# Kernel optimization log

Hardware: AMD Instinct MI355X
Metric: run time of the kernel (lower is better)

The kernel has to match this reference:

```python
import jax, jax.numpy as jnp
import numpy as np

N, E, DIN, HID, DOUT = 50000, 800000, 128, 128, 64
NEG_SLOPE = 0.2


def setup_inputs() -> dict:
    key = jax.random.key(0)
    ks = jax.random.split(key, 16)
    x = jax.random.normal(ks[0], (N, DIN), dtype=jnp.float32)
    edge_index = jax.random.randint(ks[1], (2, E), 0, N, dtype=jnp.int64)

    def lin(k, fan_in, fan_out):
        kw, kb = jax.random.split(k)
        s = 1.0 / np.sqrt(fan_in)
        W = jax.random.uniform(kw, (fan_in, fan_out), jnp.float32, -s, s)
        b = jax.random.uniform(kb, (fan_out,), jnp.float32, -s, s)
        return W, b

    Wl, bl = lin(ks[2], DIN, DIN)   # GATv2 lin_l
    Wr, br = lin(ks[3], DIN, DIN)   # GATv2 lin_r
    att = jax.random.uniform(ks[4], (DIN,), jnp.float32, -1.0 / np.sqrt(DIN), 1.0 / np.sqrt(DIN))
    bg = jnp.zeros((DIN,), jnp.float32)  # GAT output bias
    W1, b1 = lin(ks[5], DIN, HID)   # ChebConv K=1 -> plain linear
    W2, b2 = lin(ks[6], HID, HID)
    W3, b3 = lin(ks[7], HID, DOUT)
    return {"x": x, "edge_index": edge_index, "Wl": Wl, "bl": bl, "Wr": Wr,
            "br": br, "att": att, "bg": bg, "W1": W1, "b1": b1,
            "W2": W2, "b2": b2, "W3": W3, "b3": b3}


def reference(x, edge_index, Wl, bl, Wr, br, att, bg, W1, b1, W2, b2, W3, b3):
    n = x.shape[0]
    # GATv2Conv adds self loops by default
    loop = jnp.arange(n, dtype=edge_index.dtype)
    src = jnp.concatenate([edge_index[0], loop])  # source j
    dst = jnp.concatenate([edge_index[1], loop])  # target i

    xl = x @ Wl + bl  # [N, DIN]
    xr = x @ Wr + br  # [N, DIN]

    # GATv2 edge scores: leaky_relu(x_l[j] + x_r[i]) . att
    e = jax.nn.leaky_relu(xl[src] + xr[dst], NEG_SLOPE)  # [E+N, DIN]
    a = e @ att                                          # [E+N]

    # softmax over incoming edges of each destination node
    amax = jax.ops.segment_max(a, dst, num_segments=n)
    ea = jnp.exp(a - amax[dst])
    denom = jax.ops.segment_sum(ea, dst, num_segments=n)
    alpha = ea / denom[dst]                              # [E+N]

    # aggregate messages alpha * x_l[j] at destinations
    h = jax.ops.segment_sum(alpha[:, None] * xl[src], dst, num_segments=n) + bg

    # ChebConv with K=1 reduces to a linear layer (T_0(L) = I)
    h = jax.nn.relu(h @ W1 + b1)
    h = jax.nn.relu(h @ W2 + b2)
    # dropout_rate = 0.0 -> identity
    return h @ W3 + b3
```

## Files before the change

### kernel.cpp

```cpp
#include <hip/hip_runtime.h>
#include <hip/hip_bf16.h>

#define DIN 128
#define NEG_SLOPE 0.2f
#define PTILE 4096
#define PAD 64
#define SPAD 4608
#define CVT_BLKS 289

typedef __attribute__((ext_vector_type(8))) short bf16x8;
typedef __attribute__((ext_vector_type(8))) unsigned short u16x8;
typedef __attribute__((ext_vector_type(4))) float f32x4;
typedef __attribute__((ext_vector_type(2))) float f32x2;
typedef __attribute__((ext_vector_type(4))) unsigned int u32x4;

__device__ __forceinline__ ushort f2bf(float f) {
  unsigned u = __float_as_uint(f);
  u += 0x7FFFu + ((u >> 16) & 1u);
  return (ushort)(u >> 16);
}
__device__ __forceinline__ float bf2f(ushort u) {
  return __uint_as_float((unsigned)u << 16);
}
__device__ __forceinline__ f32x2 bfpair(unsigned u) {
  f32x2 r;
  r.x = __uint_as_float(u << 16);
  r.y = __uint_as_float(u & 0xFFFF0000u);
  return r;
}

template <int CTRL>
__device__ __forceinline__ float dppadd(float x) {
  int v = __builtin_amdgcn_update_dpp(0, __float_as_int(x), CTRL, 0xf, 0xf, true);
  return x + __int_as_float(v);
}
__device__ __forceinline__ float red16(float t) {
  t = dppadd<0xB1>(t);
  t = dppadd<0x4E>(t);
  t = dppadd<0x141>(t);
  t = dppadd<0x140>(t);
  return t;
}

__global__ __launch_bounds__(256) void part_cvt_kernel(
    const int* __restrict__ ei, unsigned* __restrict__ part,
    int* __restrict__ cnt2, int ntile, int E,
    const float* __restrict__ Wl, const float* __restrict__ Wr,
    const float* __restrict__ W1, const float* __restrict__ W2,
    const float* __restrict__ W3,
    ushort* __restrict__ WlT, ushort* __restrict__ WrT,
    ushort* __restrict__ W1T, ushort* __restrict__ W2T,
    ushort* __restrict__ W3T) {
  if ((int)blockIdx.x < ntile) {
    __shared__ int hist[256], pref[256], sexcl[256], curs[256];
    __shared__ unsigned buf[PTILE];
    const int tid = threadIdx.x;
    const int t = blockIdx.x;
    const int tile0 = t * PTILE;
    const int tcount = min(PTILE, E - tile0);
    hist[tid] = 0;
    __syncthreads();
    unsigned pk[PTILE / 256];
    int cnt = 0;
    for (int i = tid; i < tcount; i += 256) {
      int s = ei[tile0 + i], d = ei[E + tile0 + i];
      unsigned p = ((unsigned)d << 16) | (unsigned)s;
      pk[cnt++] = p;
      atomicAdd(&hist[d >> 8], 1);
    }
    __syncthreads();
    int v = hist[tid];
    pref[tid] = v;
    __syncthreads();
    for (int d = 1; d < 256; d <<= 1) {
      int tt = (tid >= d) ? pref[tid - d] : 0;
      __syncthreads();
      pref[tid] += tt;
      __syncthreads();
    }
    int exc = pref[tid] - v;
    sexcl[tid] = exc;
    curs[tid] = exc;
    cnt2[tid * ntile + t] = v;
    __syncthreads();
    for (int j = 0; j < cnt; j++) {
      int b = pk[j] >> 24;
      int pos = atomicAdd(&curs[b], 1);
      buf[pos] = pk[j];
    }
    __syncthreads();
    for (int i = tid; i < tcount; i += 256) {
      unsigned p = buf[i];
      int b = p >> 24;
      int r = i - sexcl[b];
      if (r < PAD)
        part[((long)b * ntile + t) * PAD + r] = p;
    }
  } else {
    int i = ((int)blockIdx.x - ntile) * 256 + threadIdx.x;
    if (i < 16384) {
      int k = i >> 7, c = i & 127; WlT[c * 128 + k] = f2bf(Wl[i]);
    } else if (i < 32768) {
      int j = i - 16384; int k = j >> 7, c = j & 127; WrT[c * 128 + k] = f2bf(Wr[j]);
    } else if (i < 49152) {
      int j = i - 32768; int k = j >> 7, c = j & 127; W1T[c * 128 + k] = f2bf(W1[j]);
    } else if (i < 65536) {
      int j = i - 49152; int k = j >> 7, c = j & 127; W2T[c * 128 + k] = f2bf(W2[j]);
    } else if (i < 73728) {
      int j = i - 65536; int k = j >> 6, c = j & 63; W3T[c * 128 + k] = f2bf(W3[j]);
    }
  }
}

#define XSP 136
__global__ __launch_bounds__(1024) void lin_fine_kernel(
    const float* __restrict__ x, const float* __restrict__ att,
    const ushort* __restrict__ WlT, const float* __restrict__ bl,
    const ushort* __restrict__ WrT, const float* __restrict__ br,
    ushort* __restrict__ xl, ushort* __restrict__ xr,
    float* __restrict__ al, float* __restrict__ ar, int n, int nblk_gemm,
    const unsigned* __restrict__ part, const int* __restrict__ cnt2,
    int* __restrict__ offsets, ushort* __restrict__ ecnt,
    ushort* __restrict__ ssrc, int ntile, int N) {
  if ((int)blockIdx.x < nblk_gemm) {
    __shared__ ushort xs[4][32][XSP];
    const int tid1 = threadIdx.x;
    const int sub = tid1 >> 8, tid = tid1 & 255;
    const int wv = tid >> 6, lane = tid & 63;
    const int m = lane & 15, quad = lane >> 4;
    const int colbase = (wv & 1) * 64;
    const int ng = wv >> 1;
    const int nodew0 = blockIdx.x * 128 + sub * 32;
    const int srow = tid >> 3, scol = (tid & 7) * 16;
    {
      int grow = nodew0 + srow; if (grow >= n) grow = n - 1;
      const float4* xp = (const float4*)(x + (long)grow * 128 + scol);
      float4 f0 = xp[0], f1 = xp[1], f2 = xp[2], f3 = xp[3];
      u16x8 o0, o1;
      o0[0] = f2bf(f0.x); o0[1] = f2bf(f0.y); o0[2] = f2bf(f0.z); o0[3] = f2bf(f0.w);
      o0[4] = f2bf(f1.x); o0[5] = f2bf(f1.y); o0[6] = f2bf(f1.z); o0[7] = f2bf(f1.w);
      o1[0] = f2bf(f2.x); o1[1] = f2bf(f2.y); o1[2] = f2bf(f2.z); o1[3] = f2bf(f2.w);
      o1[4] = f2bf(f3.x); o1[5] = f2bf(f3.y); o1[6] = f2bf(f3.z); o1[7] = f2bf(f3.w);
      *(u16x8*)&xs[sub][srow][scol]     = o0;
      *(u16x8*)&xs[sub][srow][scol + 8] = o1;
    }
    __syncthreads();
    f32x4 accl[4], accr[4];
#pragma unroll
    for (int nt = 0; nt < 4; nt++) { accl[nt] = (f32x4){0,0,0,0}; accr[nt] = (f32x4){0,0,0,0}; }
#pragma unroll
    for (int kk = 0; kk < 4; kk++) {
      int k0 = kk * 32 + quad * 8;
      bf16x8 af = *(const bf16x8*)&xs[sub][ng * 16 + m][k0];
#pragma unroll
      for (int nt = 0; nt < 4; nt++) {
        int brow = colbase + nt * 16 + m;
        bf16x8 bl8 = *(const bf16x8*)(WlT + brow * 128 + k0);
        bf16x8 br8 = *(const bf16x8*)(WrT + brow * 128 + k0);
        accl[nt] = __builtin_amdgcn_mfma_f32_16x16x32_bf16(af, bl8, accl[nt], 0, 0, 0);
        accr[nt] = __builtin_amdgcn_mfma_f32_16x16x32_bf16(af, br8, accr[nt], 0, 0, 0);
      }
    }
    __syncthreads();
#pragma unroll
    for (int nt = 0; nt < 4; nt++) {
      int col = colbase + nt * 16 + m;
      float vb = bl[col];
#pragma unroll
      for (int r = 0; r < 4; r++)
        xs[sub][ng * 16 + quad * 4 + r][col] = f2bf(accl[nt][r] + vb);
    }
    __syncthreads();
    {
      int node = nodew0 + srow;
      u16x8 o0 = *(u16x8*)&xs[sub][srow][scol];
      u16x8 o1 = *(u16x8*)&xs[sub][srow][scol + 8];
      if (node < n) {
        *(u16x8*)(xl + (long)node * 128 + scol)     = o0;
        *(u16x8*)(xl + (long)node * 128 + scol + 8) = o1;
      }
      const float4* ap = (const float4*)(att + scol);
      float4 a0 = ap[0], a1 = ap[1], a2 = ap[2], a3 = ap[3];
      float ps = a0.x*bf2f(o0[0]) + a0.y*bf2f(o0[1]) + a0.z*bf2f(o0[2]) + a0.w*bf2f(o0[3])
               + a1.x*bf2f(o0[4]) + a1.y*bf2f(o0[5]) + a1.z*bf2f(o0[6]) + a1.w*bf2f(o0[7])
               + a2.x*bf2f(o1[0]) + a2.y*bf2f(o1[1]) + a2.z*bf2f(o1[2]) + a2.w*bf2f(o1[3])
               + a3.x*bf2f(o1[4]) + a3.y*bf2f(o1[5]) + a3.z*bf2f(o1[6]) + a3.w*bf2f(o1[7]);
      ps += __shfl_xor(ps, 1); ps += __shfl_xor(ps, 2); ps += __shfl_xor(ps, 4);
      if ((tid & 7) == 0 && node < n) al[node] = ps;
    }
    __syncthreads();
#pragma unroll
    for (int nt = 0; nt < 4; nt++) {
      int col = colbase + nt * 16 + m;
      float vb = br[col];
#pragma unroll
      for (int r = 0; r < 4; r++)
        xs[sub][ng * 16 + quad * 4 + r][col] = f2bf(accr[nt][r] + vb);
    }
    __syncthreads();
    {
      int node = nodew0 + srow;
      u16x8 o0 = *(u16x8*)&xs[sub][srow][scol];
      u16x8 o1 = *(u16x8*)&xs[sub][srow][scol + 8];
      if (node < n) {
        *(u16x8*)(xr + (long)node * 128 + scol)     = o0;
        *(u16x8*)(xr + (long)node * 128 + scol + 8) = o1;
      }
      const float4* ap = (const float4*)(att + scol);
      float4 a0 = ap[0], a1 = ap[1], a2 = ap[2], a3 = ap[3];
      float ps = a0.x*bf2f(o0[0]) + a0.y*bf2f(o0[1]) + a0.z*bf2f(o0[2]) + a0.w*bf2f(o0[3])
               + a1.x*bf2f(o0[4]) + a1.y*bf2f(o0[5]) + a1.z*bf2f(o0[6]) + a1.w*bf2f(o0[7])
               + a2.x*bf2f(o1[0]) + a2.y*bf2f(o1[1]) + a2.z*bf2f(o1[2]) + a2.w*bf2f(o1[3])
               + a3.x*bf2f(o1[4]) + a3.y*bf2f(o1[5]) + a3.z*bf2f(o1[6]) + a3.w*bf2f(o1[7]);
      ps += __shfl_xor(ps, 1); ps += __shfl_xor(ps, 2); ps += __shfl_xor(ps, 4);
      if ((tid & 7) == 0 && node < n) ar[node] = ps;
    }
  } else {
    __shared__ int cnt2s[256], hist[256], curs[256];
    const int tid = threadIdx.x;
    const int b = (int)blockIdx.x - nblk_gemm;
    if (tid < 256) {
      hist[tid] = 0;
      cnt2s[tid] = (tid < ntile) ? cnt2[b * ntile + tid] : 0;
    }
    __syncthreads();
    const long base = (long)b * ntile * PAD;
    const int nv = ntile * PAD;
    for (int v = tid; v < nv; v += 1024) {
      int t = v >> 6;
      if ((v & 63) < cnt2s[t]) {
        unsigned p = part[base + v];
        atomicAdd(&hist[(p >> 16) & 255], 1);
      }
    }
    __syncthreads();
    int v0 = (tid < 256) ? hist[tid] : 0;
    if (tid < 256) curs[tid] = v0;
    __syncthreads();
    for (int d = 1; d < 256; d <<= 1) {
      int tt = (tid >= d && tid < 256) ? curs[tid - d] : 0;
      __syncthreads();
      if (tid < 256) curs[tid] += tt;
      __syncthreads();
    }
    if (tid < 256) {
      int excl = curs[tid] - v0;
      int node = b * 256 + tid;
      if (node < N) {
        offsets[node] = b * SPAD + excl;
        ecnt[node] = (ushort)v0;
      }
      curs[tid] = b * SPAD + excl;
    }
    __syncthreads();
    for (int v = tid; v < nv; v += 1024) {
      int t = v >> 6;
      if ((v & 63) < cnt2s[t]) {
        unsigned p = part[base + v];
        int pos = atomicAdd(&curs[(p >> 16) & 255], 1);
        ssrc[pos] = (ushort)(p & 0xFFFFu);
      }
    }
  }
}

__global__ __launch_bounds__(256) void node_aggr_kernel(
    const ushort* __restrict__ xl, const ushort* __restrict__ xr,
    const float* __restrict__ att, const float* __restrict__ bg,
    const float* __restrict__ al, const float* __restrict__ ar,
    const int* __restrict__ offsets, const ushort* __restrict__ ecnt,
    const ushort* __restrict__ ssrc, ushort* __restrict__ h, int n) {
  int wave = (int)((blockIdx.x * (long)blockDim.x + threadIdx.x) >> 6);
  int lane = threadIdx.x & 63;
  if (wave >= n) return;
  const int node = wave;
  const int eg = lane >> 4, sl = lane & 15;
  const int beg = offsets[node];
  const int end = beg + (int)ecnt[node];
  const int last = end - 1;
  const ushort* __restrict__ xls = xl + sl * 8;
  int ia0 = beg + 2 * eg;
  int sa  = (int)ssrc[min(ia0, last)];
  int sb  = (int)ssrc[min(ia0 + 1, last)];
  int sa2 = (int)ssrc[min(ia0 + 8, last)];
  int sb2 = (int)ssrc[min(ia0 + 9, last)];
  u32x4 uva = *(const u32x4*)(xls + (long)sa * 128);
  u32x4 uvb = *(const u32x4*)(xls + (long)sb * 128);
  float ala = al[sa], alb = al[sb];
  const float arn = ar[node];

  f32x2 a04[4], r2[4], acc2[4];
  {
    const float4* ap = (const float4*)(att + sl * 8);
    float4 a0 = ap[0], a1 = ap[1];
    f32x2 av[4] = {{a0.x, a0.y}, {a0.z, a0.w}, {a1.x, a1.y}, {a1.z, a1.w}};
#pragma unroll
    for (int jp = 0; jp < 4; jp++) a04[jp] = 0.4f * av[jp];
  }
  u32x4 rv = *(const u32x4*)(xr + (long)node * 128 + sl * 8);
  u32x4 lv = *(const u32x4*)(xls + (long)node * 128);
  float denom;
  {
    f32x2 t2 = {0.f, 0.f};
    f32x2 l2[4];
#pragma unroll
    for (int jp = 0; jp < 4; jp++) {
      r2[jp] = bfpair(rv[jp]);
      l2[jp] = bfpair(lv[jp]);
      f32x2 v = l2[jp] + r2[jp];
      t2 += a04[jp] * __builtin_elementwise_abs(v);
    }
    float t = red16(t2.x + t2.y) + 0.6f * (al[node] + arn);
    float es = __expf(t);
    denom = (eg == 0) ? es : 0.f;
#pragma unroll
    for (int jp = 0; jp < 4; jp++)
      acc2[jp] = (eg == 0) ? es * l2[jp] : (f32x2){0.f, 0.f};
  }
  for (int p = beg; p < end; p += 8) {
    u32x4 ca = uva, cb = uvb;
    float cala = ala, calb = alb;
    int ia = p + 2 * eg;
    bool cva = ia < end, cvb = ia + 1 < end;
    uva = *(const u32x4*)(xls + (long)sa2 * 128);
    uvb = *(const u32x4*)(xls + (long)sb2 * 128);
    ala = al[sa2]; alb = al[sb2];
    int ian = p + 16 + 2 * eg;
    sa2 = (int)ssrc[min(ian, last)];
    sb2 = (int)ssrc[min(ian + 1, last)];
    f32x2 ua2[4], ub2[4];
    f32x2 ta2 = {0.f, 0.f}, tb2 = {0.f, 0.f};
#pragma unroll
    for (int jp = 0; jp < 4; jp++) {
      ua2[jp] = bfpair(ca[jp]);
      ub2[jp] = bfpair(cb[jp]);
      f32x2 va2 = ua2[jp] + r2[jp];
      f32x2 vb2 = ub2[jp] + r2[jp];
      ta2 += a04[jp] * __builtin_elementwise_abs(va2);
      tb2 += a04[jp] * __builtin_elementwise_abs(vb2);
    }
    float ta = red16(ta2.x + ta2.y) + 0.6f * (cala + arn);
    float tb = red16(tb2.x + tb2.y) + 0.6f * (calb + arn);
    float ea = cva ? __expf(ta) : 0.f;
    float eb = cvb ? __expf(tb) : 0.f;
    denom += ea + eb;
#pragma unroll
    for (int jp = 0; jp < 4; jp++)
      acc2[jp] += ea * ua2[jp] + eb * ub2[jp];
  }
#pragma unroll
  for (int jp = 0; jp < 4; jp++) {
    acc2[jp].x += __shfl_xor(acc2[jp].x, 16);
    acc2[jp].y += __shfl_xor(acc2[jp].y, 16);
    acc2[jp].x += __shfl_xor(acc2[jp].x, 32);
    acc2[jp].y += __shfl_xor(acc2[jp].y, 32);
  }
  denom += __shfl_xor(denom, 16);
  denom += __shfl_xor(denom, 32);
  if (eg == 0) {
    float inv = 1.0f / denom;
    const float4* bp = (const float4*)(bg + sl * 8);
    float4 g0 = bp[0], g1 = bp[1];
    f32x2 gv[4] = {{g0.x, g0.y}, {g0.z, g0.w}, {g1.x, g1.y}, {g1.z, g1.w}};
    u16x8 o;
#pragma unroll
    for (int jp = 0; jp < 4; jp++) {
      f32x2 hv = acc2[jp] * inv + gv[jp];
      o[2 * jp]     = f2bf(hv.x);
      o[2 * jp + 1] = f2bf(hv.y);
    }
    *(u16x8*)(h + (long)node * 128 + sl * 8) = o;
  }
}

#define LDSP 136
__global__ __launch_bounds__(256) void mlp_mfma_kernel(
    const ushort* __restrict__ hb,
    const ushort* __restrict__ W1T, const float* __restrict__ b1,
    const ushort* __restrict__ W2T, const float* __restrict__ b2,
    const ushort* __restrict__ W3T, const float* __restrict__ b3,
    float* __restrict__ out, int n) {
  __shared__ ushort hst[32][LDSP];
  __shared__ ushort act[32][LDSP];
  const int tid = threadIdx.x;
  const int wv = tid >> 6, lane = tid & 63;
  const int m = lane & 15, quad = lane >> 4;
  const int half = wv & 1, ng = wv >> 1;
  const int colbase = half * 64;
  const int nodew = blockIdx.x * 32 + ng * 16;
  {
    const int srow = tid >> 3, scol = (tid & 7) * 16;
    int grow = blockIdx.x * 32 + srow; if (grow >= n) grow = n - 1;
    u16x8 o0 = *(const u16x8*)(hb + (long)grow * 128 + scol);
    u16x8 o1 = *(const u16x8*)(hb + (long)grow * 128 + scol + 8);
    *(u16x8*)&hst[srow][scol]     = o0;
    *(u16x8*)&hst[srow][scol + 8] = o1;
  }
  __syncthreads();
  f32x4 acc[4];
#pragma unroll
  for (int nt = 0; nt < 4; nt++) acc[nt] = (f32x4){0,0,0,0};
#pragma unroll
  for (int kk = 0; kk < 4; kk++) {
    int k0 = kk * 32 + quad * 8;
    bf16x8 af = *(const bf16x8*)(&hst[ng * 16 + m][k0]);
#pragma unroll
    for (int nt = 0; nt < 4; nt++) {
      bf16x8 b8 = *(const bf16x8*)(W1T + (colbase + nt * 16 + m) * 128 + k0);
      acc[nt] = __builtin_amdgcn_mfma_f32_16x16x32_bf16(af, b8, acc[nt], 0, 0, 0);
    }
  }
#pragma unroll
  for (int nt = 0; nt < 4; nt++) {
    int col = colbase + nt * 16 + m;
    float b = b1[col];
#pragma unroll
    for (int r = 0; r < 4; r++)
      act[ng * 16 + quad * 4 + r][col] = f2bf(fmaxf(acc[nt][r] + b, 0.f));
  }
  __syncthreads();
#pragma unroll
  for (int nt = 0; nt < 4; nt++) acc[nt] = (f32x4){0,0,0,0};
#pragma unroll
  for (int kk = 0; kk < 4; kk++) {
    int k0 = kk * 32 + quad * 8;
    bf16x8 af = *(const bf16x8*)(&act[ng * 16 + m][k0]);
#pragma unroll
    for (int nt = 0; nt < 4; nt++) {
      bf16x8 b8 = *(const bf16x8*)(W2T + (colbase + nt * 16 + m) * 128 + k0);
      acc[nt] = __builtin_amdgcn_mfma_f32_16x16x32_bf16(af, b8, acc[nt], 0, 0, 0);
    }
  }
  __syncthreads();
#pragma unroll
  for (int nt = 0; nt < 4; nt++) {
    int col = colbase + nt * 16 + m;
    float b = b2[col];
#pragma unroll
    for (int r = 0; r < 4; r++)
      act[ng * 16 + quad * 4 + r][col] = f2bf(fmaxf(acc[nt][r] + b, 0.f));
  }
  __syncthreads();
  f32x4 acc3[2];
#pragma unroll
  for (int nt = 0; nt < 2; nt++) acc3[nt] = (f32x4){0,0,0,0};
#pragma unroll
  for (int kk = 0; kk < 4; kk++) {
    int k0 = kk * 32 + quad * 8;
    bf16x8 af = *(const bf16x8*)(&act[ng * 16 + m][k0]);
#pragma unroll
    for (int nt = 0; nt < 2; nt++) {
      bf16x8 b8 = *(const bf16x8*)(W3T + (half * 32 + nt * 16 + m) * 128 + k0);
      acc3[nt] = __builtin_amdgcn_mfma_f32_16x16x32_bf16(af, b8, acc3[nt], 0, 0, 0);
    }
  }
#pragma unroll
  for (int nt = 0; nt < 2; nt++) {
    int col = half * 32 + nt * 16 + m;
    float b = b3[col];
#pragma unroll
    for (int r = 0; r < 4; r++) {
      int node = nodew + quad * 4 + r;
      if (node < n) out[(long)node * 64 + col] = acc3[nt][r] + b;
    }
  }
}

extern "C" void kernel_launch(void* const* d_in, const int* in_sizes, int n_in,
                              void* d_out, int out_size, void* d_ws, size_t ws_size,
                              hipStream_t stream) {
  const float* x   = (const float*)d_in[0];
  const int*   ei  = (const int*)d_in[1];
  const float* Wl  = (const float*)d_in[2];
  const float* bl  = (const float*)d_in[3];
  const float* Wr  = (const float*)d_in[4];
  const float* br  = (const float*)d_in[5];
  const float* att = (const float*)d_in[6];
  const float* bg  = (const float*)d_in[7];
  const float* W1  = (const float*)d_in[8];
  const float* b1  = (const float*)d_in[9];
  const float* W2  = (const float*)d_in[10];
  const float* b2  = (const float*)d_in[11];
  const float* W3  = (const float*)d_in[12];
  const float* b3  = (const float*)d_in[13];
  float* out = (float*)d_out;

  const int N = in_sizes[0] / DIN;
  const int E = in_sizes[1] / 2;
  const int nbuck = (N + 255) >> 8;
  const int ntile = (E + PTILE - 1) / PTILE;

  char* ws = (char*)d_ws;
  size_t off = 0;
  auto alloc = [&](size_t bytes) {
    void* p = ws + off;
    off += (bytes + 255) & ~(size_t)255;
    return p;
  };
  int* cnt2      = (int*)alloc((size_t)256 * ntile * 4);
  int* offsets   = (int*)alloc(((size_t)N + 4) * 4);
  ushort* ecnt   = (ushort*)alloc(((size_t)N + 16) * 2);
  ushort* ssrc   = (ushort*)alloc((size_t)256 * SPAD * 2 + 256);
  ushort* xlb    = (ushort*)alloc((size_t)N * DIN * 2);
  ushort* xrb    = (ushort*)alloc((size_t)N * DIN * 2);
  float* albuf   = (float*)alloc((size_t)N * 4);
  float* arbuf   = (float*)alloc((size_t)N * 4);
  size_t part_bytes = (size_t)256 * ntile * PAD * 4;
  size_t hbf_bytes  = (size_t)N * DIN * 2;
  unsigned* part = (unsigned*)alloc(part_bytes > hbf_bytes ? part_bytes : hbf_bytes);
  ushort* hbf    = (ushort*)part;
  ushort* WlT    = (ushort*)alloc(16384 * 2);
  ushort* WrT    = (ushort*)alloc(16384 * 2);
  ushort* W1T    = (ushort*)alloc(16384 * 2);
  ushort* W2T    = (ushort*)alloc(16384 * 2);
  ushort* W3T    = (ushort*)alloc(8192 * 2);
  (void)ws_size;

  part_cvt_kernel<<<ntile + CVT_BLKS, 256, 0, stream>>>(
      ei, part, cnt2, ntile, E,
      Wl, Wr, W1, W2, W3, WlT, WrT, W1T, W2T, W3T);

  int nblk_gemm = (N + 127) / 128;
  lin_fine_kernel<<<nblk_gemm + nbuck, 1024, 0, stream>>>(
      x, att, WlT, bl, WrT, br, xlb, xrb, albuf, arbuf, N, nblk_gemm,
      part, cnt2, offsets, ecnt, ssrc, ntile, N);

  int nwblk = (N + 3) / 4;
  node_aggr_kernel<<<nwblk, 256, 0, stream>>>(xlb, xrb, att, bg,
                                              albuf, arbuf,
                                              offsets, ecnt, ssrc, hbf, N);

  int nblk32 = (N + 31) / 32;
  mlp_mfma_kernel<<<nblk32, 256, 0, stream>>>(hbf, W1T, b1, W2T, b2,
                                              W3T, b3, out, N);
}
```

Measured before the change: 234.9 us.

## Split fused linear/bucket-fine kernel into separate fine and 256-thread linear kernels

Undoes the fusion of the node-linear GEMM and the per-bucket fine sort into one 1024-thread launch. They become two kernels: a 1024-thread fine_kernel and a 256-thread lin_kernel that handles 32 nodes per block. The aim is better occupancy and scheduling for the GEMM part, which no longer carries the 1024-thread block shape or the branch divergence between roles. The cost is an extra launch and the loss of overlap between the two independent workloads.

```diff
diff --git a/kernel.cpp b/kernel.cpp
--- a/kernel.cpp
+++ b/kernel.cpp
@@ -112,155 +112,154 @@
   }
 }
 
+__global__ __launch_bounds__(1024) void fine_kernel(
+    const unsigned* __restrict__ part, const int* __restrict__ cnt2,
+    int* __restrict__ offsets, ushort* __restrict__ ecnt,
+    ushort* __restrict__ ssrc, int ntile, int N) {
+  __shared__ int cnt2s[256], hist[256], curs[256];
+  const int tid = threadIdx.x;
+  const int b = blockIdx.x;
+  if (tid < 256) {
+    hist[tid] = 0;
+    cnt2s[tid] = (tid < ntile) ? cnt2[b * ntile + tid] : 0;
+  }
+  __syncthreads();
+  const long base = (long)b * ntile * PAD;
+  const int nv = ntile * PAD;
+  for (int v = tid; v < nv; v += 1024) {
+    int t = v >> 6;
+    if ((v & 63) < cnt2s[t]) {
+      unsigned p = part[base + v];
+      atomicAdd(&hist[(p >> 16) & 255], 1);
+    }
+  }
+  __syncthreads();
+  int v0 = (tid < 256) ? hist[tid] : 0;
+  if (tid < 256) curs[tid] = v0;
+  __syncthreads();
+  for (int d = 1; d < 256; d <<= 1) {
+    int tt = (tid >= d && tid < 256) ? curs[tid - d] : 0;
+    __syncthreads();
+    if (tid < 256) curs[tid] += tt;
+    __syncthreads();
+  }
+  if (tid < 256) {
+    int excl = curs[tid] - v0;
+    int node = b * 256 + tid;
+    if (node < N) {
+      offsets[node] = b * SPAD + excl;
+      ecnt[node] = (ushort)v0;
+    }
+    curs[tid] = b * SPAD + excl;
+  }
+  __syncthreads();
+  for (int v = tid; v < nv; v += 1024) {
+    int t = v >> 6;
+    if ((v & 63) < cnt2s[t]) {
+      unsigned p = part[base + v];
+      int pos = atomicAdd(&curs[(p >> 16) & 255], 1);
+      ssrc[pos] = (ushort)(p & 0xFFFFu);
+    }
+  }
+}
+
 #define XSP 136
-__global__ __launch_bounds__(1024) void lin_fine_kernel(
+__global__ __launch_bounds__(256) void lin_kernel(
     const float* __restrict__ x, const float* __restrict__ att,
     const ushort* __restrict__ WlT, const float* __restrict__ bl,
     const ushort* __restrict__ WrT, const float* __restrict__ br,
     ushort* __restrict__ xl, ushort* __restrict__ xr,
-    float* __restrict__ al, float* __restrict__ ar, int n, int nblk_gemm,
-    const unsigned* __restrict__ part, const int* __restrict__ cnt2,
-    int* __restrict__ offsets, ushort* __restrict__ ecnt,
-    ushort* __restrict__ ssrc, int ntile, int N) {
-  if ((int)blockIdx.x < nblk_gemm) {
-    __shared__ ushort xs[4][32][XSP];
-    const int tid1 = threadIdx.x;
-    const int sub = tid1 >> 8, tid = tid1 & 255;
-    const int wv = tid >> 6, lane = tid & 63;
-    const int m = lane & 15, quad = lane >> 4;
-    const int colbase = (wv & 1) * 64;
-    const int ng = wv >> 1;
-    const int nodew0 = blockIdx.x * 128 + sub * 32;
-    const int srow = tid >> 3, scol = (tid & 7) * 16;
-    {
-      int grow = nodew0 + srow; if (grow >= n) grow = n - 1;
-      const float4* xp = (const float4*)(x + (long)grow * 128 + scol);
-      float4 f0 = xp[0], f1 = xp[1], f2 = xp[2], f3 = xp[3];
-      u16x8 o0, o1;
-      o0[0] = f2bf(f0.x); o0[1] = f2bf(f0.y); o0[2] = f2bf(f0.z); o0[3] = f2bf(f0.w);
-      o0[4] = f2bf(f1.x); o0[5] = f2bf(f1.y); o0[6] = f2bf(f1.z); o0[7] = f2bf(f1.w);
-      o1[0] = f2bf(f2.x); o1[1] = f2bf(f2.y); o1[2] = f2bf(f2.z); o1[3] = f2bf(f2.w);
-      o1[4] = f2bf(f3.x); o1[5] = f2bf(f3.y); o1[6] = f2bf(f3.z); o1[7] = f2bf(f3.w);
-      *(u16x8*)&xs[sub][srow][scol]     = o0;
-      *(u16x8*)&xs[sub][srow][scol + 8] = o1;
-    }
-    __syncthreads();
-    f32x4 accl[4], accr[4];
-#pragma unroll
-    for (int nt = 0; nt < 4; nt++) { accl[nt] = (f32x4){0,0,0,0}; accr[nt] = (f32x4){0,0,0,0}; }
-#pragma unroll
-    for (int kk = 0; kk < 4; kk++) {
-      int k0 = kk * 32 + quad * 8;
-      bf16x8 af = *(const bf16x8*)&xs[sub][ng * 16 + m][k0];
-#pragma unroll
-      for (int nt = 0; nt < 4; nt++) {
-        int brow = colbase + nt * 16 + m;
-        bf16x8 bl8 = *(const bf16x8*)(WlT + brow * 128 + k0);
-        bf16x8 br8 = *(const bf16x8*)(WrT + brow * 128 + k0);
-        accl[nt] = __builtin_amdgcn_mfma_f32_16x16x32_bf16(af, bl8, accl[nt], 0, 0, 0);
-        accr[nt] = __builtin_amdgcn_mfma_f32_16x16x32_bf16(af, br8, accr[nt], 0, 0, 0);
-      }
-    }
-    __syncthreads();
+    float* __restrict__ al, float* __restrict__ ar, int n) {
+  __shared__ ushort xs[32][XSP];
+  const int tid = threadIdx.x;
+  const int wv = tid >> 6, lane = tid & 63;
+  const int m = lane & 15, quad = lane >> 4;
+  const int colbase = (wv & 1) * 64;
+  const int ng = wv >> 1;
+  const int nodew0 = blockIdx.x * 32;
+  const int srow = tid >> 3, scol = (tid & 7) * 16;
+  {
+    int grow = nodew0 + srow; if (grow >= n) grow = n - 1;
+    const float4* xp = (const float4*)(x + (long)grow * 128 + scol);
+    float4 f0 = xp[0], f1 = xp[1], f2 = xp[2], f3 = xp[3];
+    u16x8 o0, o1;
+    o0[0] = f2bf(f0.x); o0[1] = f2bf(f0.y); o0[2] = f2bf(f0.z); o0[3] = f2bf(f0.w);
+    o0[4] = f2bf(f1.x); o0[5] = f2bf(f1.y); o0[6] = f2bf(f1.z); o0[7] = f2bf(f1.w);
+    o1[0] = f2bf(f2.x); o1[1] = f2bf(f2.y); o1[2] = f2bf(f2.z); o1[3] = f2bf(f2.w);
+    o1[4] = f2bf(f3.x); o1[5] = f2bf(f3.y); o1[6] = f2bf(f3.z); o1[7] = f2bf(f3.w);
+    *(u16x8*)&xs[srow][scol]     = o0;
+    *(u16x8*)&xs[srow][scol + 8] = o1;
+  }
+  __syncthreads();
+  f32x4 accl[4], accr[4];
+#pragma unroll
+  for (int nt = 0; nt < 4; nt++) { accl[nt] = (f32x4){0,0,0,0}; accr[nt] = (f32x4){0,0,0,0}; }
+#pragma unroll
+  for (int kk = 0; kk < 4; kk++) {
+    int k0 = kk * 32 + quad * 8;
+    bf16x8 af = *(const bf16x8*)&xs[ng * 16 + m][k0];
 #pragma unroll
     for (int nt = 0; nt < 4; nt++) {
-      int col = colbase + nt * 16 + m;
-      float vb = bl[col];
-#pragma unroll
-      for (int r = 0; r < 4; r++)
-        xs[sub][ng * 16 + quad * 4 + r][col] = f2bf(accl[nt][r] + vb);
-    }
-    __syncthreads();
-    {
-      int node = nodew0 + srow;
-      u16x8 o0 = *(u16x8*)&xs[sub][srow][scol];
-      u16x8 o1 = *(u16x8*)&xs[sub][srow][scol + 8];
-      if (node < n) {
-        *(u16x8*)(xl + (long)node * 128 + scol)     = o0;
-        *(u16x8*)(xl + (long)node * 128 + scol + 8) = o1;
-      }
-      const float4* ap = (const float4*)(att + scol);
-      float4 a0 = ap[0], a1 = ap[1], a2 = ap[2], a3 = ap[3];
-      float ps = a0.x*bf2f(o0[0]) + a0.y*bf2f(o0[1]) + a0.z*bf2f(o0[2]) + a0.w*bf2f(o0[3])
-               + a1.x*bf2f(o0[4]) + a1.y*bf2f(o0[5]) + a1.z*bf2f(o0[6]) + a1.w*bf2f(o0[7])
-               + a2.x*bf2f(o1[0]) + a2.y*bf2f(o1[1]) + a2.z*bf2f(o1[2]) + a2.w*bf2f(o1[3])
-               + a3.x*bf2f(o1[4]) + a3.y*bf2f(o1[5]) + a3.z*bf2f(o1[6]) + a3.w*bf2f(o1[7]);
-      ps += __shfl_xor(ps, 1); ps += __shfl_xor(ps, 2); ps += __shfl_xor(ps, 4);
-      if ((tid & 7) == 0 && node < n) al[node] = ps;
-    }
-    __syncthreads();
-#pragma unroll
-    for (int nt = 0; nt < 4; nt++) {
-      int col = colbase + nt * 16 + m;
-      float vb = br[col];
-#pragma unroll
-      for (int r = 0; r < 4; r++)
-        xs[sub][ng * 16 + quad * 4 + r][col] = f2bf(accr[nt][r] + vb);
-    }
-    __syncthreads();
-    {
-      int node = nodew0 + srow;
-      u16x8 o0 = *(u16x8*)&xs[sub][srow][scol];
-      u16x8 o1 = *(u16x8*)&xs[sub][srow][scol + 8];
-      if (node < n) {
-        *(u16x8*)(xr + (long)node * 128 + scol)     = o0;
-        *(u16x8*)(xr + (long)node * 128 + scol + 8) = o1;
-      }
-      const float4* ap = (const float4*)(att + scol);
-      float4 a0 = ap[0], a1 = ap[1], a2 = ap[2], a3 = ap[3];
-      float ps = a0.x*bf2f(o0[0]) + a0.y*bf2f(o0[1]) + a0.z*bf2f(o0[2]) + a0.w*bf2f(o0[3])
-               + a1.x*bf2f(o0[4]) + a1.y*bf2f(o0[5]) + a1.z*bf2f(o0[6]) + a1.w*bf2f(o0[7])
-               + a2.x*bf2f(o1[0]) + a2.y*bf2f(o1[1]) + a2.z*bf2f(o1[2]) + a2.w*bf2f(o1[3])
-               + a3.x*bf2f(o1[4]) + a3.y*bf2f(o1[5]) + a3.z*bf2f(o1[6]) + a3.w*bf2f(o1[7]);
-      ps += __shfl_xor(ps, 1); ps += __shfl_xor(ps, 2); ps += __shfl_xor(ps, 4);
-      if ((tid & 7) == 0 && node < n) ar[node] = ps;
-    }
-  } else {
-    __shared__ int cnt2s[256], hist[256], curs[256];
-    const int tid = threadIdx.x;
-    const int b = (int)blockIdx.x - nblk_gemm;
-    if (tid < 256) {
-      hist[tid] = 0;
-      cnt2s[tid] = (tid < ntile) ? cnt2[b * ntile + tid] : 0;
-    }
-    __syncthreads();
-    const long base = (long)b * ntile * PAD;
-    const int nv = ntile * PAD;
-    for (int v = tid; v < nv; v += 1024) {
-      int t = v >> 6;
-      if ((v & 63) < cnt2s[t]) {
-        unsigned p = part[base + v];
-        atomicAdd(&hist[(p >> 16) & 255], 1);
-      }
-    }
-    __syncthreads();
-    int v0 = (tid < 256) ? hist[tid] : 0;
-    if (tid < 256) curs[tid] = v0;
-    __syncthreads();
-    for (int d = 1; d < 256; d <<= 1) {
-      int tt = (tid >= d && tid < 256) ? curs[tid - d] : 0;
-      __syncthreads();
-      if (tid < 256) curs[tid] += tt;
-      __syncthreads();
-    }
-    if (tid < 256) {
-      int excl = curs[tid] - v0;
-      int node = b * 256 + tid;
-      if (node < N) {
-        offsets[node] = b * SPAD + excl;
-        ecnt[node] = (ushort)v0;
-      }
-      curs[tid] = b * SPAD + excl;
-    }
-    __syncthreads();
-    for (int v = tid; v < nv; v += 1024) {
-      int t = v >> 6;
-      if ((v & 63) < cnt2s[t]) {
-        unsigned p = part[base + v];
-        int pos = atomicAdd(&curs[(p >> 16) & 255], 1);
-        ssrc[pos] = (ushort)(p & 0xFFFFu);
-      }
-    }
+      int brow = colbase + nt * 16 + m;
+      bf16x8 bl8 = *(const bf16x8*)(WlT + brow * 128 + k0);
+      bf16x8 br8 = *(const bf16x8*)(WrT + brow * 128 + k0);
+      accl[nt] = __builtin_amdgcn_mfma_f32_16x16x32_bf16(af, bl8, accl[nt], 0, 0, 0);
+      accr[nt] = __builtin_amdgcn_mfma_f32_16x16x32_bf16(af, br8, accr[nt], 0, 0, 0);
+    }
+  }
+  __syncthreads();
+#pragma unroll
+  for (int nt = 0; nt < 4; nt++) {
+    int col = colbase + nt * 16 + m;
+    float vb = bl[col];
+#pragma unroll
+    for (int r = 0; r < 4; r++)
+      xs[ng * 16 + quad * 4 + r][col] = f2bf(accl[nt][r] + vb);
+  }
+  __syncthreads();
+  {
+    int node = nodew0 + srow;
+    u16x8 o0 = *(u16x8*)&xs[srow][scol];
+    u16x8 o1 = *(u16x8*)&xs[srow][scol + 8];
+    if (node < n) {
+      *(u16x8*)(xl + (long)node * 128 + scol)     = o0;
+      *(u16x8*)(xl + (long)node * 128 + scol + 8) = o1;
+    }
+    const float4* ap = (const float4*)(att + scol);
+    float4 a0 = ap[0], a1 = ap[1], a2 = ap[2], a3 = ap[3];
+    float ps = a0.x*bf2f(o0[0]) + a0.y*bf2f(o0[1]) + a0.z*bf2f(o0[2]) + a0.w*bf2f(o0[3])
+             + a1.x*bf2f(o0[4]) + a1.y*bf2f(o0[5]) + a1.z*bf2f(o0[6]) + a1.w*bf2f(o0[7])
+             + a2.x*bf2f(o1[0]) + a2.y*bf2f(o1[1]) + a2.z*bf2f(o1[2]) + a2.w*bf2f(o1[3])
+             + a3.x*bf2f(o1[4]) + a3.y*bf2f(o1[5]) + a3.z*bf2f(o1[6]) + a3.w*bf2f(o1[7]);
+    ps += __shfl_xor(ps, 1); ps += __shfl_xor(ps, 2); ps += __shfl_xor(ps, 4);
+    if ((tid & 7) == 0 && node < n) al[node] = ps;
+  }
+  __syncthreads();
+#pragma unroll
+  for (int nt = 0; nt < 4; nt++) {
+    int col = colbase + nt * 16 + m;
+    float vb = br[col];
+#pragma unroll
+    for (int r = 0; r < 4; r++)
+      xs[ng * 16 + quad * 4 + r][col] = f2bf(accr[nt][r] + vb);
+  }
+  __syncthreads();
+  {
+    int node = nodew0 + srow;
+    u16x8 o0 = *(u16x8*)&xs[srow][scol];
+    u16x8 o1 = *(u16x8*)&xs[srow][scol + 8];
+    if (node < n) {
+      *(u16x8*)(xr + (long)node * 128 + scol)     = o0;
+      *(u16x8*)(xr + (long)node * 128 + scol + 8) = o1;
+    }
+    const float4* ap = (const float4*)(att + scol);
+    float4 a0 = ap[0], a1 = ap[1], a2 = ap[2], a3 = ap[3];
+    float ps = a0.x*bf2f(o0[0]) + a0.y*bf2f(o0[1]) + a0.z*bf2f(o0[2]) + a0.w*bf2f(o0[3])
+             + a1.x*bf2f(o0[4]) + a1.y*bf2f(o0[5]) + a1.z*bf2f(o0[6]) + a1.w*bf2f(o0[7])
+             + a2.x*bf2f(o1[0]) + a2.y*bf2f(o1[1]) + a2.z*bf2f(o1[2]) + a2.w*bf2f(o1[3])
+             + a3.x*bf2f(o1[4]) + a3.y*bf2f(o1[5]) + a3.z*bf2f(o1[6]) + a3.w*bf2f(o1[7]);
+    ps += __shfl_xor(ps, 1); ps += __shfl_xor(ps, 2); ps += __shfl_xor(ps, 4);
+    if ((tid & 7) == 0 && node < n) ar[node] = ps;
   }
 }
 
@@ -520,17 +519,18 @@
       ei, part, cnt2, ntile, E,
       Wl, Wr, W1, W2, W3, WlT, WrT, W1T, W2T, W3T);
 
-  int nblk_gemm = (N + 127) / 128;
-  lin_fine_kernel<<<nblk_gemm + nbuck, 1024, 0, stream>>>(
-      x, att, WlT, bl, WrT, br, xlb, xrb, albuf, arbuf, N, nblk_gemm,
-      part, cnt2, offsets, ecnt, ssrc, ntile, N);
+  fine_kernel<<<nbuck, 1024, 0, stream>>>(part, cnt2, offsets, ecnt,
+                                          ssrc, ntile, N);
+
+  int nblk32 = (N + 31) / 32;
+  lin_kernel<<<nblk32, 256, 0, stream>>>(x, att, WlT, bl, WrT, br,
+                                         xlb, xrb, albuf, arbuf, N);
 
   int nwblk = (N + 3) / 4;
   node_aggr_kernel<<<nwblk, 256, 0, stream>>>(xlb, xrb, att, bg,
                                               albuf, arbuf,
                                               offsets, ecnt, ssrc, hbf, N);
 
-  int nblk32 = (N + 31) / 32;
   mlp_mfma_kernel<<<nblk32, 256, 0, stream>>>(hbf, W1T, b1, W2T, b2,
                                               W3T, b3, out, N);
 }
```

Result: slower. 243.0 us (+3.5%).
